# Optimization experiments

Measured on AMD Instinct MI355X. Metric: run time of the kernel, lower is better.

## Reference

```python
import jax, jax.numpy as jnp
import numpy as np

INPUT_SIZE = 64
HIDDEN = 512
BATCH = 256
SEQ = 512

def _rnn_layer(x, W_ih, W_hh, b_ih, b_hh):
    # x: (B, T, D_in). PyTorch RNN step: h_t = tanh(x_t W_ih^T + b_ih + h_{t-1} W_hh^T + b_hh)
    B = x.shape[0]
    # precompute input projections for all timesteps: (B, T, H)
    xp = jnp.einsum('btd,hd->bth', x, W_ih) + b_ih + b_hh
    h0 = jnp.zeros((B, W_hh.shape[0]), dtype=x.dtype)

    def step(h, xp_t):
        h_new = jnp.tanh(xp_t + h @ W_hh.T)
        return h_new, h_new

    _, hs = jax.lax.scan(step, h0, jnp.swapaxes(xp, 0, 1))  # hs: (T, B, H)
    return jnp.swapaxes(hs, 0, 1)  # (B, T, H)

def setup_inputs() -> dict:
    key = jax.random.key(0)
    ks = jax.random.split(key, 11)
    s_in = 1.0 / np.sqrt(HIDDEN)
    u = lambda k, shape: jax.random.uniform(k, shape, jnp.float32, -s_in, s_in)
    return {
        'x': jax.random.normal(ks[0], (BATCH, SEQ, INPUT_SIZE), jnp.float32),
        'W_ih0': u(ks[1], (HIDDEN, INPUT_SIZE)),
        'W_hh0': u(ks[2], (HIDDEN, HIDDEN)),
        'b_ih0': u(ks[3], (HIDDEN,)),
        'b_hh0': u(ks[4], (HIDDEN,)),
        'W_ih1': u(ks[5], (HIDDEN, HIDDEN)),
        'W_hh1': u(ks[6], (HIDDEN, HIDDEN)),
        'b_ih1': u(ks[7], (HIDDEN,)),
        'b_hh1': u(ks[8], (HIDDEN,)),
        'W_fc': u(ks[9], (1, HIDDEN)),
        'b_fc': u(ks[10], (1,)),
    }

def reference(x, W_ih0, W_hh0, b_ih0, b_hh0, W_ih1, W_hh1, b_ih1, b_hh1, W_fc, b_fc):
    h1 = _rnn_layer(x, W_ih0, W_hh0, b_ih0, b_hh0)   # (B, T, H)
    h2 = _rnn_layer(h1, W_ih1, W_hh1, b_ih1, b_hh1)  # (B, T, H)
    last = h2[:, -1, :]                              # (B, H)
    return last @ W_fc.T + b_fc                      # (B, 1)
```

## Files before the change

kernel.cpp:

```cpp
#include <hip/hip_runtime.h>
#include <hip/hip_fp16.h>


typedef _Float16 h2 __attribute__((ext_vector_type(2)));
typedef _Float16 h8 __attribute__((ext_vector_type(8)));
typedef float    f4 __attribute__((ext_vector_type(4)));

#define HID   512
#define TSEQ  512
#define NB    256
#define NWAVE 8
#define NAG   32
#define NVG   14
#define NREGF (NAG + NVG)
#define NLDSF 18

#define MFMA_A(accv, av, bv) \
  asm("v_mfma_f32_16x16x32_f16 %0, %1, %2, %0" : "+v"(accv) : "v"(av), "a"(bv))
#define MFMA_V(accv, av, bv) \
  asm("v_mfma_f32_16x16x32_f16 %0, %1, %2, %0" : "+v"(accv) : "v"(av), "v"(bv))

static const size_t OFF_P   = 0;
static const size_t OFF_B0  = 134217728;
static const size_t OFF_B1  = OFF_B0 + 65536;
static const size_t OFF_R0  = OFF_B1 + 524288;
static const size_t OFF_L0  = OFF_R0 + 376832;
static const size_t OFF_R1  = OFF_L0 + 147456;
static const size_t OFF_L1  = OFF_R1 + 376832;
static const size_t OFF_BS0 = OFF_L1 + 147456;
static const size_t OFF_BS1 = OFF_BS0 + 2048;

__global__ void bias_kernel(const float* __restrict__ bih0, const float* __restrict__ bhh0,
                            const float* __restrict__ bih1, const float* __restrict__ bhh1,
                            float* __restrict__ bias0, float* __restrict__ bias1) {
  int i = threadIdx.x;
  bias0[i] = bih0[i] + bhh0[i];
  bias1[i] = bih1[i] + bhh1[i];
}

__global__ void cvt_half_kernel(const float* __restrict__ in, _Float16* __restrict__ outp, int n) {
  int i = blockIdx.x * 256 + threadIdx.x;
  if (i < n) outp[i] = (_Float16)in[i];
}

__global__ void pack_rec_kernel(const float* __restrict__ W, uint4* __restrict__ BregP,
                                uint4* __restrict__ BldsP) {
  int t = blockIdx.x * 256 + threadIdx.x;
  int l  = t & 63;
  int g  = (t >> 6) & 3;
  int kk = (t >> 8) & 15;
  int w  = (t >> 12) & 7;
  int n  = 64 * w + 16 * g + (l & 15);
  int k0 = 32 * kk + ((l >> 4) & 3) * 8;
  const float* src = W + (size_t)n * HID + k0;
  h8 v;
#pragma unroll
  for (int i = 0; i < 8; ++i) v[i] = (_Float16)src[i];
  uint4 u = __builtin_bit_cast(uint4, v);
  if (g < 2) {
    BregP[(w * NREGF + 2 * kk + g) * 64 + l] = u;
  } else if (g == 2) {
    if (kk < 14) BregP[(w * NREGF + NAG + kk) * 64 + l] = u;
    else         BldsP[(w * NLDSF + 16 + (kk - 14)) * 64 + l] = u;
  } else {
    BldsP[(w * NLDSF + kk) * 64 + l] = u;
  }
}

template <typename AT, int K>
__global__ __launch_bounds__(256, 2) void proj_kernel(const AT* A, const _Float16* __restrict__ Bw,
                                                      _Float16* C, const float* __restrict__ bias) {
  __shared__ _Float16 At[64][40];
  __shared__ _Float16 Bt[512][40];
  const int tid = threadIdx.x;
  const int m0 = blockIdx.x * 64;
  const int wv = tid >> 6;
  const int l = tid & 63;
  const int n0 = wv * 128;
  const int lm = l & 15;
  const int lq = l >> 4;

  f4 acc[4][8];
#pragma unroll
  for (int i = 0; i < 4; ++i)
#pragma unroll
    for (int j = 0; j < 8; ++j) acc[i][j] = (f4){0.f, 0.f, 0.f, 0.f};

  const int arow = tid >> 2;
  const int kq = (tid & 3) * 8;

  for (int k0 = 0; k0 < K; k0 += 32) {
    if (sizeof(AT) == 4) {
      const float* ap = (const float*)A + (size_t)(m0 + arow) * K + k0 + kq;
      h8 v;
#pragma unroll
      for (int i = 0; i < 8; ++i) v[i] = (_Float16)ap[i];
      *(h8*)&At[arow][kq] = v;
    } else {
      *(h8*)&At[arow][kq] = *(const h8*)((const _Float16*)A + (size_t)(m0 + arow) * K + k0 + kq);
    }
#pragma unroll
    for (int rr = 0; rr < 8; ++rr) {
      int rrow = arow + rr * 64;
      *(h8*)&Bt[rrow][kq] = *(const h8*)(Bw + (size_t)rrow * K + k0 + kq);
    }
    __syncthreads();
    h8 af[4];
#pragma unroll
    for (int mm = 0; mm < 4; ++mm) af[mm] = *(const h8*)&At[mm * 16 + lm][lq * 8];
#pragma unroll
    for (int nn = 0; nn < 8; ++nn) {
      h8 bf = *(const h8*)&Bt[n0 + nn * 16 + lm][lq * 8];
#pragma unroll
      for (int mm = 0; mm < 4; ++mm)
        acc[mm][nn] = __builtin_amdgcn_mfma_f32_16x16x32_f16(af[mm], bf, acc[mm][nn], 0, 0, 0);
    }
    __syncthreads();
  }
#pragma unroll
  for (int nn = 0; nn < 8; ++nn) {
    int col = n0 + nn * 16 + lm;
    float bv = bias[col];
#pragma unroll
    for (int mm = 0; mm < 4; ++mm) {
#pragma unroll
      for (int r = 0; r < 4; ++r) {
        int row = m0 + mm * 16 + lq * 4 + r;
        C[(size_t)row * HID + col] = (_Float16)(acc[mm][nn][r] + bv);
      }
    }
  }
}

template <bool WRITE_H, bool DO_FC>
__global__ __launch_bounds__(512, 2) void rec_kernel(
    const _Float16* __restrict__ P, _Float16* __restrict__ Pout,
    const uint4* __restrict__ BregP, const uint4* __restrict__ BldsP,
    const float* __restrict__ Wfc, const float* __restrict__ bfc, float* __restrict__ out) {
  __shared__ __align__(16) uint4 Blds[NWAVE * NLDSF * 64];
  __shared__ __align__(16) _Float16 hbuf[2][HID];
  __shared__ __align__(16) float hxch[NWAVE][64];
  __shared__ float red[NWAVE];
  const int tid = threadIdx.x;
  const int b = blockIdx.x;
  const int w = tid >> 6, l = tid & 63, lq = l >> 4;

  h8 breg_a[NAG];
#pragma unroll
  for (int i = 0; i < NAG; ++i)
    breg_a[i] = __builtin_bit_cast(h8, BregP[(w * NREGF + i) * 64 + l]);
  h8 breg_v[NVG];
#pragma unroll
  for (int i = 0; i < NVG; ++i)
    breg_v[i] = __builtin_bit_cast(h8, BregP[(w * NREGF + NAG + i) * 64 + l]);
#pragma unroll
  for (int j = 0; j < NLDSF; ++j)
    Blds[(w * NLDSF + j) * 64 + l] = BldsP[(w * NLDSF + j) * 64 + l];

  ((unsigned short*)hbuf[0])[tid] = 0;
  __syncthreads();

  const _Float16* prow = P + (size_t)b * TSEQ * HID;
  unsigned short xp_cur = *(const unsigned short*)(prow + tid);
  float lv = 0.f;

#pragma unroll 1
  for (int t = 0; t < TSEQ; ++t) {
    int tn = (t + 1 < TSEQ) ? t + 1 : t;
    unsigned short xp_next = *(const unsigned short*)(prow + (size_t)tn * HID + tid);
    const _Float16* hb = hbuf[t & 1];

    f4 acc[4];
#pragma unroll
    for (int g = 0; g < 4; ++g) acc[g] = (f4){0.f, 0.f, 0.f, 0.f};

#pragma unroll
    for (int kk = 0; kk < 16; ++kk) {
      h8 a = *(const h8*)(hb + kk * 32 + lq * 8);
      MFMA_A(acc[0], a, breg_a[2 * kk]);
      MFMA_A(acc[1], a, breg_a[2 * kk + 1]);
      if (kk < 14) {
        MFMA_V(acc[2], a, breg_v[kk]);
      } else {
        h8 bf = __builtin_bit_cast(h8, Blds[(w * NLDSF + 16 + (kk - 14)) * 64 + l]);
        MFMA_V(acc[2], a, bf);
      }
      {
        h8 bf = __builtin_bit_cast(h8, Blds[(w * NLDSF + kk) * 64 + l]);
        MFMA_V(acc[3], a, bf);
      }
    }

    if (l < 16) {
#pragma unroll
      for (int g = 0; g < 4; ++g) hxch[w][16 * g + l] = acc[g][0];
    }
    asm volatile("s_waitcnt lgkmcnt(0)" ::: "memory");
    float hr = hxch[w][l];

    float v = tanhf(hr + (float)__builtin_bit_cast(_Float16, xp_cur));
    lv = v;
    _Float16 hw = (_Float16)v;
    *(_Float16*)(&hbuf[(t + 1) & 1][tid]) = hw;
    if (WRITE_H)
      *(Pout + (size_t)b * TSEQ * HID + (size_t)t * HID + tid) = hw;
    __syncthreads();
    xp_cur = xp_next;
  }

  if (DO_FC) {
    float fc = lv * Wfc[tid];
#pragma unroll
    for (int off = 32; off; off >>= 1) fc += __shfl_down(fc, off, 64);
    if (l == 0) red[w] = fc;
    __syncthreads();
    if (tid == 0) {
      float s = bfc[0];
#pragma unroll
      for (int i = 0; i < NWAVE; ++i) s += red[i];
      out[b] = s;
    }
  }
}

extern "C" void kernel_launch(void* const* d_in, const int* in_sizes, int n_in,
                              void* d_out, int out_size, void* d_ws, size_t ws_size,
                              hipStream_t stream) {
  const float* x    = (const float*)d_in[0];
  const float* Wih0 = (const float*)d_in[1];
  const float* Whh0 = (const float*)d_in[2];
  const float* bih0 = (const float*)d_in[3];
  const float* bhh0 = (const float*)d_in[4];
  const float* Wih1 = (const float*)d_in[5];
  const float* Whh1 = (const float*)d_in[6];
  const float* bih1 = (const float*)d_in[7];
  const float* bhh1 = (const float*)d_in[8];
  const float* Wfc  = (const float*)d_in[9];
  const float* bfc  = (const float*)d_in[10];
  float* out = (float*)d_out;
  char* ws = (char*)d_ws;

  _Float16* P  = (_Float16*)(ws + OFF_P);
  _Float16* B0 = (_Float16*)(ws + OFF_B0);
  _Float16* B1 = (_Float16*)(ws + OFF_B1);
  uint4* R0 = (uint4*)(ws + OFF_R0);
  uint4* L0 = (uint4*)(ws + OFF_L0);
  uint4* R1 = (uint4*)(ws + OFF_R1);
  uint4* L1 = (uint4*)(ws + OFF_L1);
  float* bias0 = (float*)(ws + OFF_BS0);
  float* bias1 = (float*)(ws + OFF_BS1);

  bias_kernel<<<1, 512, 0, stream>>>(bih0, bhh0, bih1, bhh1, bias0, bias1);
  cvt_half_kernel<<<128, 256, 0, stream>>>(Wih0, B0, 512 * 64);
  cvt_half_kernel<<<1024, 256, 0, stream>>>(Wih1, B1, 512 * 512);
  pack_rec_kernel<<<128, 256, 0, stream>>>(Whh0, R0, L0);
  pack_rec_kernel<<<128, 256, 0, stream>>>(Whh1, R1, L1);

  proj_kernel<float, 64><<<2048, 256, 0, stream>>>(x, B0, P, bias0);
  rec_kernel<true, false><<<NB, 512, 0, stream>>>(P, P, R0, L0, nullptr, nullptr, nullptr);
  proj_kernel<_Float16, 512><<<2048, 256, 0, stream>>>(P, B1, P, bias1);
  rec_kernel<false, true><<<NB, 512, 0, stream>>>(P, nullptr, R1, L1, Wfc, bfc, out);
}
```

Before: 1.641 ms.

## Rotate K order per wave so own h slice starts MFMAs before barrier

```diff
diff --git a/kernel.cpp b/kernel.cpp
--- a/kernel.cpp
+++ b/kernel.cpp
@@ -10,10 +10,8 @@
 #define TSEQ  512
 #define NB    256
 #define NWAVE 8
-#define NAG   32
-#define NVG   14
-#define NREGF (NAG + NVG)
-#define NLDSF 18
+#define NRSL  46
+#define NLSL  18
 
 #define MFMA_A(accv, av, bv) \
   asm("v_mfma_f32_16x16x32_f16 %0, %1, %2, %0" : "+v"(accv) : "v"(av), "a"(bv))
@@ -50,6 +48,7 @@
   int g  = (t >> 6) & 3;
   int kk = (t >> 8) & 15;
   int w  = (t >> 12) & 7;
+  int j  = (kk - 2 * w) & 15;
   int n  = 64 * w + 16 * g + (l & 15);
   int k0 = 32 * kk + ((l >> 4) & 3) * 8;
   const float* src = W + (size_t)n * HID + k0;
@@ -58,12 +57,12 @@
   for (int i = 0; i < 8; ++i) v[i] = (_Float16)src[i];
   uint4 u = __builtin_bit_cast(uint4, v);
   if (g < 2) {
-    BregP[(w * NREGF + 2 * kk + g) * 64 + l] = u;
+    BregP[(w * NRSL + 2 * j + g) * 64 + l] = u;
   } else if (g == 2) {
-    if (kk < 14) BregP[(w * NREGF + NAG + kk) * 64 + l] = u;
-    else         BldsP[(w * NLDSF + 16 + (kk - 14)) * 64 + l] = u;
+    if (j < 14) BregP[(w * NRSL + 32 + j) * 64 + l] = u;
+    else        BldsP[(w * NLSL + 16 + (j - 14)) * 64 + l] = u;
   } else {
-    BldsP[(w * NLDSF + kk) * 64 + l] = u;
+    BldsP[(w * NLSL + j) * 64 + l] = u;
   }
 }
 
@@ -137,63 +136,97 @@
     const _Float16* __restrict__ P, _Float16* __restrict__ Pout,
     const uint4* __restrict__ BregP, const uint4* __restrict__ BldsP,
     const float* __restrict__ Wfc, const float* __restrict__ bfc, float* __restrict__ out) {
-  __shared__ __align__(16) uint4 Blds[NWAVE * NLDSF * 64];
-  __shared__ __align__(16) _Float16 hbuf[2][HID];
+  __shared__ __align__(16) uint4 Blds[NWAVE * NLSL * 64];
+  __shared__ __align__(16) _Float16 hbuf2[2][2 * HID];
   __shared__ __align__(16) float hxch[NWAVE][64];
   __shared__ float red[NWAVE];
   const int tid = threadIdx.x;
   const int b = blockIdx.x;
   const int w = tid >> 6, l = tid & 63, lq = l >> 4;
 
-  h8 breg_a[NAG];
-#pragma unroll
-  for (int i = 0; i < NAG; ++i)
-    breg_a[i] = __builtin_bit_cast(h8, BregP[(w * NREGF + i) * 64 + l]);
-  h8 breg_v[NVG];
-#pragma unroll
-  for (int i = 0; i < NVG; ++i)
-    breg_v[i] = __builtin_bit_cast(h8, BregP[(w * NREGF + NAG + i) * 64 + l]);
-#pragma unroll
-  for (int j = 0; j < NLDSF; ++j)
-    Blds[(w * NLDSF + j) * 64 + l] = BldsP[(w * NLDSF + j) * 64 + l];
-
-  ((unsigned short*)hbuf[0])[tid] = 0;
+  h8 breg_a[32];
+#pragma unroll
+  for (int i = 0; i < 32; ++i)
+    breg_a[i] = __builtin_bit_cast(h8, BregP[(w * NRSL + i) * 64 + l]);
+  h8 breg_v[14];
+#pragma unroll
+  for (int i = 0; i < 14; ++i)
+    breg_v[i] = __builtin_bit_cast(h8, BregP[(w * NRSL + 32 + i) * 64 + l]);
+  const uint4* bl = &Blds[w * NLSL * 64 + l];
+#pragma unroll
+  for (int s = 0; s < NLSL; ++s)
+    Blds[(w * NLSL + s) * 64 + l] = BldsP[(w * NLSL + s) * 64 + l];
+
+  hbuf2[0][tid] = (_Float16)0.f;
+  hbuf2[0][tid + 512] = (_Float16)0.f;
   __syncthreads();
 
   const _Float16* prow = P + (size_t)b * TSEQ * HID;
+  _Float16* pw = WRITE_H ? (Pout + (size_t)b * TSEQ * HID + tid) : nullptr;
   unsigned short xp_cur = *(const unsigned short*)(prow + tid);
+  const int abase = 64 * w + 8 * lq;
   float lv = 0.f;
+
+  f4 acc0, acc1, acc2, acc3;
+
+  acc0 = (f4){0.f, 0.f, 0.f, 0.f}; acc1 = acc0; acc2 = acc0; acc3 = acc0;
+  {
+    const _Float16* hbn = hbuf2[0];
+    h8 A0 = *(const h8*)(hbn + abase);
+    h8 A1 = *(const h8*)(hbn + abase + 32);
+    h8 bf0 = __builtin_bit_cast(h8, bl[0 * 64]);
+    h8 bf1 = __builtin_bit_cast(h8, bl[1 * 64]);
+    MFMA_A(acc0, A0, breg_a[0]); MFMA_A(acc1, A0, breg_a[1]);
+    MFMA_V(acc2, A0, breg_v[0]); MFMA_V(acc3, A0, bf0);
+    MFMA_A(acc0, A1, breg_a[2]); MFMA_A(acc1, A1, breg_a[3]);
+    MFMA_V(acc2, A1, breg_v[1]); MFMA_V(acc3, A1, bf1);
+  }
 
 #pragma unroll 1
   for (int t = 0; t < TSEQ; ++t) {
+    __syncthreads();
     int tn = (t + 1 < TSEQ) ? t + 1 : t;
     unsigned short xp_next = *(const unsigned short*)(prow + (size_t)tn * HID + tid);
-    const _Float16* hb = hbuf[t & 1];
-
-    f4 acc[4];
-#pragma unroll
-    for (int g = 0; g < 4; ++g) acc[g] = (f4){0.f, 0.f, 0.f, 0.f};
-
-#pragma unroll
-    for (int kk = 0; kk < 16; ++kk) {
-      h8 a = *(const h8*)(hb + kk * 32 + lq * 8);
-      MFMA_A(acc[0], a, breg_a[2 * kk]);
-      MFMA_A(acc[1], a, breg_a[2 * kk + 1]);
-      if (kk < 14) {
-        MFMA_V(acc[2], a, breg_v[kk]);
-      } else {
-        h8 bf = __builtin_bit_cast(h8, Blds[(w * NLDSF + 16 + (kk - 14)) * 64 + l]);
-        MFMA_V(acc[2], a, bf);
-      }
-      {
-        h8 bf = __builtin_bit_cast(h8, Blds[(w * NLDSF + kk) * 64 + l]);
-        MFMA_V(acc[3], a, bf);
-      }
-    }
+    const _Float16* hb = hbuf2[t & 1];
+
+#define AFRAG(J) (*(const h8*)(hb + abase + 32 * (J)))
+#define LDSF(S) __builtin_bit_cast(h8, bl[(S) * 64])
+    { h8 A = AFRAG(2);  MFMA_A(acc0, A, breg_a[4]);  MFMA_A(acc1, A, breg_a[5]);
+      MFMA_V(acc2, A, breg_v[2]);  h8 bf = LDSF(2);  MFMA_V(acc3, A, bf); }
+    { h8 A = AFRAG(3);  MFMA_A(acc0, A, breg_a[6]);  MFMA_A(acc1, A, breg_a[7]);
+      MFMA_V(acc2, A, breg_v[3]);  h8 bf = LDSF(3);  MFMA_V(acc3, A, bf); }
+    { h8 A = AFRAG(4);  MFMA_A(acc0, A, breg_a[8]);  MFMA_A(acc1, A, breg_a[9]);
+      MFMA_V(acc2, A, breg_v[4]);  h8 bf = LDSF(4);  MFMA_V(acc3, A, bf); }
+    { h8 A = AFRAG(5);  MFMA_A(acc0, A, breg_a[10]); MFMA_A(acc1, A, breg_a[11]);
+      MFMA_V(acc2, A, breg_v[5]);  h8 bf = LDSF(5);  MFMA_V(acc3, A, bf); }
+    { h8 A = AFRAG(6);  MFMA_A(acc0, A, breg_a[12]); MFMA_A(acc1, A, breg_a[13]);
+      MFMA_V(acc2, A, breg_v[6]);  h8 bf = LDSF(6);  MFMA_V(acc3, A, bf); }
+    { h8 A = AFRAG(7);  MFMA_A(acc0, A, breg_a[14]); MFMA_A(acc1, A, breg_a[15]);
+      MFMA_V(acc2, A, breg_v[7]);  h8 bf = LDSF(7);  MFMA_V(acc3, A, bf); }
+    { h8 A = AFRAG(8);  MFMA_A(acc0, A, breg_a[16]); MFMA_A(acc1, A, breg_a[17]);
+      MFMA_V(acc2, A, breg_v[8]);  h8 bf = LDSF(8);  MFMA_V(acc3, A, bf); }
+    { h8 A = AFRAG(9);  MFMA_A(acc0, A, breg_a[18]); MFMA_A(acc1, A, breg_a[19]);
+      MFMA_V(acc2, A, breg_v[9]);  h8 bf = LDSF(9);  MFMA_V(acc3, A, bf); }
+    { h8 A = AFRAG(10); MFMA_A(acc0, A, breg_a[20]); MFMA_A(acc1, A, breg_a[21]);
+      MFMA_V(acc2, A, breg_v[10]); h8 bf = LDSF(10); MFMA_V(acc3, A, bf); }
+    { h8 A = AFRAG(11); MFMA_A(acc0, A, breg_a[22]); MFMA_A(acc1, A, breg_a[23]);
+      MFMA_V(acc2, A, breg_v[11]); h8 bf = LDSF(11); MFMA_V(acc3, A, bf); }
+    { h8 A = AFRAG(12); MFMA_A(acc0, A, breg_a[24]); MFMA_A(acc1, A, breg_a[25]);
+      MFMA_V(acc2, A, breg_v[12]); h8 bf = LDSF(12); MFMA_V(acc3, A, bf); }
+    { h8 A = AFRAG(13); MFMA_A(acc0, A, breg_a[26]); MFMA_A(acc1, A, breg_a[27]);
+      MFMA_V(acc2, A, breg_v[13]); h8 bf = LDSF(13); MFMA_V(acc3, A, bf); }
+    { h8 A = AFRAG(14); MFMA_A(acc0, A, breg_a[28]); MFMA_A(acc1, A, breg_a[29]);
+      h8 b2 = LDSF(16); MFMA_V(acc2, A, b2); h8 b3 = LDSF(14); MFMA_V(acc3, A, b3); }
+    { h8 A = AFRAG(15); MFMA_A(acc0, A, breg_a[30]); MFMA_A(acc1, A, breg_a[31]);
+      h8 b2 = LDSF(17); MFMA_V(acc2, A, b2); h8 b3 = LDSF(15); MFMA_V(acc3, A, b3); }
+#undef AFRAG
+#undef LDSF
 
     if (l < 16) {
-#pragma unroll
-      for (int g = 0; g < 4; ++g) hxch[w][16 * g + l] = acc[g][0];
+      hxch[w][l]      = acc0[0];
+      hxch[w][16 + l] = acc1[0];
+      hxch[w][32 + l] = acc2[0];
+      hxch[w][48 + l] = acc3[0];
     }
     asm volatile("s_waitcnt lgkmcnt(0)" ::: "memory");
     float hr = hxch[w][l];
@@ -201,10 +234,23 @@
     float v = tanhf(hr + (float)__builtin_bit_cast(_Float16, xp_cur));
     lv = v;
     _Float16 hw = (_Float16)v;
-    *(_Float16*)(&hbuf[(t + 1) & 1][tid]) = hw;
-    if (WRITE_H)
-      *(Pout + (size_t)b * TSEQ * HID + (size_t)t * HID + tid) = hw;
-    __syncthreads();
+    _Float16* hbn = hbuf2[(t + 1) & 1];
+    hbn[tid] = hw;
+    hbn[tid + 512] = hw;
+    if (WRITE_H) pw[(size_t)t * HID] = hw;
+    asm volatile("s_waitcnt lgkmcnt(0)" ::: "memory");
+
+    acc0 = (f4){0.f, 0.f, 0.f, 0.f}; acc1 = acc0; acc2 = acc0; acc3 = acc0;
+    {
+      h8 A0 = *(const h8*)(hbn + abase);
+      h8 A1 = *(const h8*)(hbn + abase + 32);
+      h8 bf0 = __builtin_bit_cast(h8, bl[0 * 64]);
+      h8 bf1 = __builtin_bit_cast(h8, bl[1 * 64]);
+      MFMA_A(acc0, A0, breg_a[0]); MFMA_A(acc1, A0, breg_a[1]);
+      MFMA_V(acc2, A0, breg_v[0]); MFMA_V(acc3, A0, bf0);
+      MFMA_A(acc0, A1, breg_a[2]); MFMA_A(acc1, A1, breg_a[3]);
+      MFMA_V(acc2, A1, breg_v[1]); MFMA_V(acc3, A1, bf1);
+    }
     xp_cur = xp_next;
   }
 
```

Result: no change. 1.643 ms (+0.1%).
